# Optimization experiments

Measured on AMD Instinct MI355X. Metric: run time of the kernel, lower is better.

The kernel has to match this reference:

```python
import jax, jax.numpy as jnp
import numpy as np
from jax import lax

S, L = 8192, 16
N_WORD, N_CHAR = 50000, 128
WORD_DIM, CHAR_DIM = 256, 64
WORD_HID, CHAR_HID = 512, 128
N_TAG = 64


def _lstm_gates(x, h, Wih, Whh, bih, bhh):
    # x: [..., D], h: [..., H]; torch gate order: i, f, g, o
    g = x @ Wih.T + h @ Whh.T + bih + bhh
    i, f, gg, o = jnp.split(g, 4, axis=-1)
    return jax.nn.sigmoid(i), jax.nn.sigmoid(f), jnp.tanh(gg), jax.nn.sigmoid(o)


def setup_inputs() -> dict:
    key = jax.random.key(0)
    ks = jax.random.split(key, 16)
    sc = 0.1
    inp = {
        'x': jax.random.randint(ks[0], (S,), 0, N_WORD),
        'chars': jax.random.randint(ks[1], (S, L), 0, N_CHAR),
        'lengths': jax.random.randint(ks[2], (S,), 0, L),
        'word_emb': jax.random.normal(ks[3], (N_WORD, WORD_DIM), jnp.float32) * sc,
        'char_emb': jax.random.normal(ks[4], (N_CHAR, CHAR_DIM), jnp.float32) * sc,
        'c_Wih': jax.random.normal(ks[5], (4 * CHAR_HID, CHAR_DIM), jnp.float32) * sc,
        'c_Whh': jax.random.normal(ks[6], (4 * CHAR_HID, CHAR_HID), jnp.float32) * sc,
        'c_bih': jax.random.normal(ks[7], (4 * CHAR_HID,), jnp.float32) * sc,
        'c_bhh': jax.random.normal(ks[8], (4 * CHAR_HID,), jnp.float32) * sc,
        'w_Wih': jax.random.normal(ks[9], (4 * WORD_HID, WORD_DIM + CHAR_HID), jnp.float32) * sc,
        'w_Whh': jax.random.normal(ks[10], (4 * WORD_HID, WORD_HID), jnp.float32) * sc,
        'w_bih': jax.random.normal(ks[11], (4 * WORD_HID,), jnp.float32) * sc,
        'w_bhh': jax.random.normal(ks[12], (4 * WORD_HID,), jnp.float32) * sc,
        'lin_W': jax.random.normal(ks[13], (N_TAG, WORD_HID), jnp.float32) * sc,
        'lin_b': jax.random.normal(ks[14], (N_TAG,), jnp.float32) * sc,
    }
    return inp


def _char_features(chars, lengths, char_emb, Wih, Whh, bih, bhh):
    # batched char LSTM over all S words at once; returns final CELL state (h[1] in torch)
    emb = char_emb[chars]              # [S, L, char_dim]
    xs = jnp.swapaxes(emb, 0, 1)       # [L, S, char_dim]
    h0 = jnp.zeros((chars.shape[0], CHAR_HID), emb.dtype)
    c0 = jnp.zeros_like(h0)

    def step(carry, inp):
        h, c = carry
        x_t, t = inp
        i, f, g, o = _lstm_gates(x_t, h, Wih, Whh, bih, bhh)
        c_new = f * c + i * g
        h_new = o * jnp.tanh(c_new)
        m = (t < lengths)[:, None]     # only update within each word's true length
        return (jnp.where(m, h_new, h), jnp.where(m, c_new, c)), None

    (h, c), _ = lax.scan(step, (h0, c0), (xs, jnp.arange(L)))
    return c                            # [S, char_hidden]


def _word_lstm(seq, Wih, Whh, bih, bhh):
    # seq: [S, D] single sequence (batch=1 in original)
    h0 = jnp.zeros((WORD_HID,), seq.dtype)
    c0 = jnp.zeros_like(h0)

    def step(carry, x_t):
        h, c = carry
        i, f, g, o = _lstm_gates(x_t, h, Wih, Whh, bih, bhh)
        c = f * c + i * g
        h = o * jnp.tanh(c)
        return (h, c), h

    _, hs = lax.scan(step, (h0, c0), seq)
    return hs                           # [S, word_hidden]


def reference(x, chars, lengths, word_emb, char_emb,
              c_Wih, c_Whh, c_bih, c_bhh,
              w_Wih, w_Whh, w_bih, w_bhh,
              lin_W, lin_b):
    char_feat = _char_features(chars, lengths, char_emb, c_Wih, c_Whh, c_bih, c_bhh)
    we = word_emb[x]                                    # [S, word_dim]
    seq = jnp.concatenate([we, char_feat], axis=1)      # [S, word_dim+char_hidden]
    hs = _word_lstm(seq, w_Wih, w_Whh, w_bih, w_bhh)    # [S, word_hidden]
    logits = hs @ lin_W.T + lin_b                       # [S, n_tag]
    return jax.nn.log_softmax(logits, axis=1)
```

## Files before the change

kernel.cpp:

```cpp
#include <hip/hip_runtime.h>
#include <hip/hip_bf16.h>

#define S_LEN 8192
#define CLEN 16
#define WDIM 256
#define CDIM 64
#define CHID 128
#define WHID 512
#define GDIM 2048
#define NTAG 64
#define KDIM 384
#define NWG 32

typedef unsigned long long u64;

__device__ __forceinline__ float sigmoidf_(float x) {
  return 1.0f / (1.0f + __expf(-x));
}
__device__ __forceinline__ float tanhf_(float x) {
  return 1.0f - 2.0f / (__expf(2.0f * x) + 1.0f);
}

__global__ __launch_bounds__(256)
void char_lstm_kernel(const int* __restrict__ chars, const int* __restrict__ lengths,
                      const float* __restrict__ emb, const float* __restrict__ Wih,
                      const float* __restrict__ Whh, const float* __restrict__ bih,
                      const float* __restrict__ bhh, float* __restrict__ cf)
{
  __shared__ float xs[16][CDIM];
  __shared__ float hsm[16][CHID];
  __shared__ int cidx[16];
  __shared__ int lens[16];
  const int tid = threadIdx.x;
  const int grp = tid >> 7;
  const int j = tid & 127;
  const int wb = blockIdx.x * 16;

  for (int i = tid; i < 16 * CHID; i += 256) (&hsm[0][0])[i] = 0.f;
  if (tid < 16) lens[tid] = lengths[wb + tid];
  float c[8];
#pragma unroll
  for (int w = 0; w < 8; ++w) c[w] = 0.f;
  const float bi = bih[j] + bhh[j];
  const float bf = bih[CHID + j] + bhh[CHID + j];
  const float bg = bih[2 * CHID + j] + bhh[2 * CHID + j];
  const float bo = bih[3 * CHID + j] + bhh[3 * CHID + j];

  for (int t = 0; t < CLEN; ++t) {
    __syncthreads();
    if (tid < 16) cidx[tid] = chars[(wb + tid) * CLEN + t];
    __syncthreads();
    {
      int e = tid * 4;
      int wi = e >> 6;
      int k = e & 63;
      const float4 v = *(const float4*)(emb + (size_t)cidx[wi] * CDIM + k);
      *(float4*)(&xs[wi][k]) = v;
    }
    __syncthreads();
    float ai[8], af[8], ag[8], ao[8];
#pragma unroll
    for (int w = 0; w < 8; ++w) { ai[w] = bi; af[w] = bf; ag[w] = bg; ao[w] = bo; }
    for (int k = 0; k < CDIM; k += 4) {
      float4 w0 = *(const float4*)(Wih + (size_t)j * CDIM + k);
      float4 w1 = *(const float4*)(Wih + (size_t)(CHID + j) * CDIM + k);
      float4 w2 = *(const float4*)(Wih + (size_t)(2 * CHID + j) * CDIM + k);
      float4 w3 = *(const float4*)(Wih + (size_t)(3 * CHID + j) * CDIM + k);
#pragma unroll
      for (int s = 0; s < 4; ++s) {
        float wiv = (&w0.x)[s], wfv = (&w1.x)[s], wgv = (&w2.x)[s], wov = (&w3.x)[s];
#pragma unroll
        for (int w = 0; w < 8; ++w) {
          float xv = xs[grp * 8 + w][k + s];
          ai[w] = fmaf(wiv, xv, ai[w]);
          af[w] = fmaf(wfv, xv, af[w]);
          ag[w] = fmaf(wgv, xv, ag[w]);
          ao[w] = fmaf(wov, xv, ao[w]);
        }
      }
    }
    for (int k = 0; k < CHID; k += 4) {
      float4 w0 = *(const float4*)(Whh + (size_t)j * CHID + k);
      float4 w1 = *(const float4*)(Whh + (size_t)(CHID + j) * CHID + k);
      float4 w2 = *(const float4*)(Whh + (size_t)(2 * CHID + j) * CHID + k);
      float4 w3 = *(const float4*)(Whh + (size_t)(3 * CHID + j) * CHID + k);
#pragma unroll
      for (int s = 0; s < 4; ++s) {
        float wiv = (&w0.x)[s], wfv = (&w1.x)[s], wgv = (&w2.x)[s], wov = (&w3.x)[s];
#pragma unroll
        for (int w = 0; w < 8; ++w) {
          float hv = hsm[grp * 8 + w][k + s];
          ai[w] = fmaf(wiv, hv, ai[w]);
          af[w] = fmaf(wfv, hv, af[w]);
          ag[w] = fmaf(wgv, hv, ag[w]);
          ao[w] = fmaf(wov, hv, ao[w]);
        }
      }
    }
    __syncthreads();
#pragma unroll
    for (int w = 0; w < 8; ++w) {
      if (t < lens[grp * 8 + w]) {
        float iv = sigmoidf_(ai[w]);
        float fv = sigmoidf_(af[w]);
        float gv = tanhf_(ag[w]);
        float ov = sigmoidf_(ao[w]);
        c[w] = fv * c[w] + iv * gv;
        hsm[grp * 8 + w][j] = ov * tanhf_(c[w]);
      }
    }
  }
#pragma unroll
  for (int w = 0; w < 8; ++w)
    cf[(size_t)(wb + grp * 8 + w) * CHID + j] = c[w];
}

#define BM 64
#define BN 64
#define BK 32
__global__ __launch_bounds__(256)
void gx_gemm_kernel(const int* __restrict__ x, const float* __restrict__ word_emb,
                    const float* __restrict__ char_feat, const float* __restrict__ Wih,
                    const float* __restrict__ bih, const float* __restrict__ bhh,
                    float* __restrict__ Gx)
{
  __shared__ float As[BK][BM + 1];
  __shared__ float Bs[BK][BN + 1];
  __shared__ int xidx[BM];
  const int tid = threadIdx.x;
  const int tx = tid & 15, ty = tid >> 4;
  const int m0 = blockIdx.y * BM;
  const int n0 = blockIdx.x * BN;
  if (tid < BM) xidx[tid] = x[m0 + tid];
  float acc[4][4] = {};
  for (int k0 = 0; k0 < KDIM; k0 += BK) {
    __syncthreads();
    {
      int i = tid >> 5;
      int kk = tid & 31;
#pragma unroll
      for (int l = 0; l < 8; ++l) {
        int row = i + l * 8;
        int k = k0 + kk;
        int tt = m0 + row;
        float v = (k < WDIM) ? word_emb[(size_t)xidx[row] * WDIM + k]
                             : char_feat[(size_t)tt * CHID + (k - WDIM)];
        As[kk][row] = v;
      }
    }
    {
      int jjj = tid >> 5;
      int kk = tid & 31;
#pragma unroll
      for (int l = 0; l < 8; ++l) {
        int col = jjj + l * 8;
        Bs[kk][col] = Wih[(size_t)(n0 + col) * KDIM + k0 + kk];
      }
    }
    __syncthreads();
#pragma unroll
    for (int kk = 0; kk < BK; ++kk) {
      float a[4], b[4];
#pragma unroll
      for (int m = 0; m < 4; ++m) a[m] = As[kk][ty * 4 + m];
#pragma unroll
      for (int n = 0; n < 4; ++n) b[n] = Bs[kk][tx * 4 + n];
#pragma unroll
      for (int m = 0; m < 4; ++m)
#pragma unroll
        for (int n = 0; n < 4; ++n)
          acc[m][n] = fmaf(a[m], b[n], acc[m][n]);
    }
  }
#pragma unroll
  for (int n = 0; n < 4; ++n) {
    int g = n0 + tx * 4 + n;
    float bias = bih[g] + bhh[g];
#pragma unroll
    for (int m = 0; m < 4; ++m) {
      int tt = m0 + ty * 4 + m;
      Gx[(size_t)tt * GDIM + g] = acc[m][n] + bias;
    }
  }
}

__global__ __launch_bounds__(256, 1)
void word_lstm_seq(const float* __restrict__ Whh, const float* __restrict__ Gx,
                   float* __restrict__ hs, u64* hbuf)
{
  extern __shared__ float4 wlds4[];
  __shared__ float h_lds[WHID];
  __shared__ float red[2][256];
  const int tid  = threadIdx.x;
  const int wg   = blockIdx.x;
  const int cc   = tid >> 6;
  const int lane = tid & 63;
  const int kb   = cc * 128;
  const int grow = (lane >> 4) * WHID + wg * 16 + (lane & 15);

  for (int L = tid; L < 8192; L += 256) {
    int c2  = L >> 11;
    int rem = L & 2047;
    int j   = rem >> 6;
    int r   = rem & 63;
    int gr  = (r >> 4) * WHID + wg * 16 + (r & 15);
    wlds4[L] = *(const float4*)(Whh + (size_t)gr * WHID + c2 * 128 + 4 * j);
  }
  __syncthreads();

  float c_state = 0.f;

  for (int t = 0; t < S_LEN; ++t) {
    const int par = t & 1;
    float gxv = 0.f;
    if (tid < 64)
      gxv = Gx[(size_t)t * GDIM + grow];
    float v0 = 0.f, v1 = 0.f;
    if (t > 0) {
      const u64* ps = hbuf + (size_t)par * WHID + kb + 2 * lane;
      const unsigned want = (unsigned)t;
      u64 a, b;
      do {
        a = __hip_atomic_load(ps + 0, __ATOMIC_RELAXED, __HIP_MEMORY_SCOPE_AGENT);
        b = __hip_atomic_load(ps + 1, __ATOMIC_RELAXED, __HIP_MEMORY_SCOPE_AGENT);
      } while (((unsigned)(a >> 32) != want) | ((unsigned)(b >> 32) != want));
      v0 = __uint_as_float((unsigned)a);
      v1 = __uint_as_float((unsigned)b);
    }
    *(float2*)(&h_lds[kb + 2 * lane]) = make_float2(v0, v1);
    __threadfence_block();
    const float4* wp = wlds4 + cc * 2048;
    float acc = 0.f;
#pragma unroll
    for (int j = 0; j < 32; ++j) {
      const float4 wv = wp[j * 64 + lane];
      const float4 hv = *(const float4*)(&h_lds[kb + 4 * j]);
      acc = fmaf(wv.x, hv.x, acc);
      acc = fmaf(wv.y, hv.y, acc);
      acc = fmaf(wv.z, hv.z, acc);
      acc = fmaf(wv.w, hv.w, acc);
    }
    red[par][tid] = acc;
    __syncthreads();
    if (tid < 64) {
      const float* rp = red[par];
      float s = rp[tid] + rp[64 + tid] + rp[128 + tid] + rp[192 + tid] + gxv;
      float act = ((tid >> 4) == 2) ? tanhf_(s) : sigmoidf_(s);
      int jj = tid & 15;
      float iv = __shfl(act, jj);
      float fv = __shfl(act, 16 + jj);
      float gv = __shfl(act, 32 + jj);
      float ov = __shfl(act, 48 + jj);
      if (tid < 16) {
        c_state = fv * c_state + iv * gv;
        float hv = ov * tanhf_(c_state);
        const int hidx = wg * 16 + tid;
        const u64 pkt = ((u64)(unsigned)(t + 1) << 32) | (u64)__float_as_uint(hv);
        (void)__hip_atomic_exchange(&hbuf[(size_t)((t + 1) & 1) * WHID + hidx],
                                    pkt, __ATOMIC_RELAXED,
                                    __HIP_MEMORY_SCOPE_AGENT);
        hs[(size_t)t * WHID + hidx] = hv;
      }
    }
  }
}

__global__ __launch_bounds__(256)
void tag_kernel(const float* __restrict__ hs, const float* __restrict__ W,
                const float* __restrict__ b, float* __restrict__ out)
{
  const int wave = threadIdx.x >> 6;
  const int lane = threadIdx.x & 63;
  const int t = blockIdx.x * 4 + wave;
  const float* hr = hs + (size_t)t * WHID;
  const float* wr = W + (size_t)lane * WHID;
  float acc = b[lane];
  for (int k = 0; k < WHID; k += 4) {
    float4 wv = *(const float4*)(wr + k);
    float4 hv = *(const float4*)(hr + k);
    acc = fmaf(wv.x, hv.x, acc);
    acc = fmaf(wv.y, hv.y, acc);
    acc = fmaf(wv.z, hv.z, acc);
    acc = fmaf(wv.w, hv.w, acc);
  }
  float m = acc;
#pragma unroll
  for (int off = 32; off > 0; off >>= 1) m = fmaxf(m, __shfl_xor(m, off));
  float e = __expf(acc - m);
  float sum = e;
#pragma unroll
  for (int off = 32; off > 0; off >>= 1) sum += __shfl_xor(sum, off);
  out[(size_t)t * NTAG + lane] = (acc - m) - __logf(sum);
}

extern "C" void kernel_launch(void* const* d_in, const int* in_sizes, int n_in,
                              void* d_out, int out_size, void* d_ws, size_t ws_size,
                              hipStream_t stream)
{
  const int* x          = (const int*)d_in[0];
  const int* chars      = (const int*)d_in[1];
  const int* lengths    = (const int*)d_in[2];
  const float* word_emb = (const float*)d_in[3];
  const float* char_emb = (const float*)d_in[4];
  const float* c_Wih    = (const float*)d_in[5];
  const float* c_Whh    = (const float*)d_in[6];
  const float* c_bih    = (const float*)d_in[7];
  const float* c_bhh    = (const float*)d_in[8];
  const float* w_Wih    = (const float*)d_in[9];
  const float* w_Whh    = (const float*)d_in[10];
  const float* w_bih    = (const float*)d_in[11];
  const float* w_bhh    = (const float*)d_in[12];
  const float* lin_W    = (const float*)d_in[13];
  const float* lin_b    = (const float*)d_in[14];
  float* out = (float*)d_out;

  char* ws = (char*)d_ws;
  u64*   hbuf      = (u64*)ws;
  float* char_feat = (float*)(ws + 8192);
  float* Gx        = (float*)(ws + 8192 + (size_t)S_LEN * CHID * 4);
  float* hs        = (float*)(ws + 8192 + (size_t)S_LEN * CHID * 4
                                        + (size_t)S_LEN * GDIM * 4);

  hipMemsetAsync(ws, 0, 8192, stream);

  char_lstm_kernel<<<S_LEN / 16, 256, 0, stream>>>(
      chars, lengths, char_emb, c_Wih, c_Whh, c_bih, c_bhh, char_feat);

  dim3 g2(GDIM / BN, S_LEN / BM);
  gx_gemm_kernel<<<g2, 256, 0, stream>>>(
      x, word_emb, char_feat, w_Wih, w_bih, w_bhh, Gx);

  hipFuncSetAttribute((const void*)word_lstm_seq,
                      hipFuncAttributeMaxDynamicSharedMemorySize, 131072);
  word_lstm_seq<<<NWG, 256, 131072, stream>>>(w_Whh, Gx, hs, hbuf);

  tag_kernel<<<S_LEN / 4, 256, 0, stream>>>(hs, lin_W, lin_b, out);
}
```

Before: 17.10 ms.

## Fuse input projection into word LSTM recurrence with register-resident weights

Removes the separate Gx GEMM kernel and its large intermediate buffer. The sequential word LSTM kernel now computes the input projection per timestep itself, gathering the word embedding and char feature into LDS. Both Whh and Wih slices are held in registers (224 floats per thread) instead of LDS. This avoids a full GEMM plus the Gx write/read, but adds per-step global loads and extra FMAs on the serial critical path, and risks register spills.

```diff
diff --git a/kernel.cpp b/kernel.cpp
--- a/kernel.cpp
+++ b/kernel.cpp
@@ -115,106 +115,52 @@
     cf[(size_t)(wb + grp * 8 + w) * CHID + j] = c[w];
 }
 
-#define BM 64
-#define BN 64
-#define BK 32
-__global__ __launch_bounds__(256)
-void gx_gemm_kernel(const int* __restrict__ x, const float* __restrict__ word_emb,
-                    const float* __restrict__ char_feat, const float* __restrict__ Wih,
-                    const float* __restrict__ bih, const float* __restrict__ bhh,
-                    float* __restrict__ Gx)
-{
-  __shared__ float As[BK][BM + 1];
-  __shared__ float Bs[BK][BN + 1];
-  __shared__ int xidx[BM];
-  const int tid = threadIdx.x;
-  const int tx = tid & 15, ty = tid >> 4;
-  const int m0 = blockIdx.y * BM;
-  const int n0 = blockIdx.x * BN;
-  if (tid < BM) xidx[tid] = x[m0 + tid];
-  float acc[4][4] = {};
-  for (int k0 = 0; k0 < KDIM; k0 += BK) {
-    __syncthreads();
-    {
-      int i = tid >> 5;
-      int kk = tid & 31;
-#pragma unroll
-      for (int l = 0; l < 8; ++l) {
-        int row = i + l * 8;
-        int k = k0 + kk;
-        int tt = m0 + row;
-        float v = (k < WDIM) ? word_emb[(size_t)xidx[row] * WDIM + k]
-                             : char_feat[(size_t)tt * CHID + (k - WDIM)];
-        As[kk][row] = v;
-      }
-    }
-    {
-      int jjj = tid >> 5;
-      int kk = tid & 31;
-#pragma unroll
-      for (int l = 0; l < 8; ++l) {
-        int col = jjj + l * 8;
-        Bs[kk][col] = Wih[(size_t)(n0 + col) * KDIM + k0 + kk];
-      }
-    }
-    __syncthreads();
-#pragma unroll
-    for (int kk = 0; kk < BK; ++kk) {
-      float a[4], b[4];
-#pragma unroll
-      for (int m = 0; m < 4; ++m) a[m] = As[kk][ty * 4 + m];
-#pragma unroll
-      for (int n = 0; n < 4; ++n) b[n] = Bs[kk][tx * 4 + n];
-#pragma unroll
-      for (int m = 0; m < 4; ++m)
-#pragma unroll
-        for (int n = 0; n < 4; ++n)
-          acc[m][n] = fmaf(a[m], b[n], acc[m][n]);
-    }
-  }
-#pragma unroll
-  for (int n = 0; n < 4; ++n) {
-    int g = n0 + tx * 4 + n;
-    float bias = bih[g] + bhh[g];
-#pragma unroll
-    for (int m = 0; m < 4; ++m) {
-      int tt = m0 + ty * 4 + m;
-      Gx[(size_t)tt * GDIM + g] = acc[m][n] + bias;
-    }
-  }
-}
-
 __global__ __launch_bounds__(256, 1)
-void word_lstm_seq(const float* __restrict__ Whh, const float* __restrict__ Gx,
+void word_lstm_seq(const float* __restrict__ Whh, const float* __restrict__ Wih,
+                   const float* __restrict__ bih, const float* __restrict__ bhh,
+                   const int* __restrict__ x, const float* __restrict__ word_emb,
+                   const float* __restrict__ cf,
                    float* __restrict__ hs, u64* hbuf)
 {
-  extern __shared__ float4 wlds4[];
   __shared__ float h_lds[WHID];
+  __shared__ float x_lds[KDIM];
   __shared__ float red[2][256];
   const int tid  = threadIdx.x;
   const int wg   = blockIdx.x;
   const int cc   = tid >> 6;
   const int lane = tid & 63;
   const int kb   = cc * 128;
+  const int xb   = cc * 96;
   const int grow = (lane >> 4) * WHID + wg * 16 + (lane & 15);
 
-  for (int L = tid; L < 8192; L += 256) {
-    int c2  = L >> 11;
-    int rem = L & 2047;
-    int j   = rem >> 6;
-    int r   = rem & 63;
-    int gr  = (r >> 4) * WHID + wg * 16 + (r & 15);
-    wlds4[L] = *(const float4*)(Whh + (size_t)gr * WHID + c2 * 128 + 4 * j);
-  }
-  __syncthreads();
+  float wl[128];
+  {
+    const float* wsrc = Whh + (size_t)grow * WHID + kb;
+#pragma unroll
+    for (int k = 0; k < 128; ++k) wl[k] = wsrc[k];
+  }
+  float wx[96];
+  {
+    const float* wsrc = Wih + (size_t)grow * KDIM + xb;
+#pragma unroll
+    for (int k = 0; k < 96; ++k) wx[k] = wsrc[k];
+  }
+  const float bias = bih[grow] + bhh[grow];
 
   float c_state = 0.f;
 
   for (int t = 0; t < S_LEN; ++t) {
     const int par = t & 1;
-    float gxv = 0.f;
-    if (tid < 64)
-      gxv = Gx[(size_t)t * GDIM + grow];
+    {
+      const int xt = x[t];
+      if (lane < 24) {
+        const int gk = xb + 4 * lane;
+        float4 v = (gk < WDIM)
+            ? *(const float4*)(word_emb + (size_t)xt * WDIM + gk)
+            : *(const float4*)(cf + (size_t)t * CHID + (gk - WDIM));
+        *(float4*)(&x_lds[gk]) = v;
+      }
+    }
     float v0 = 0.f, v1 = 0.f;
     if (t > 0) {
       const u64* ps = hbuf + (size_t)par * WHID + kb + 2 * lane;
@@ -229,22 +175,28 @@
     }
     *(float2*)(&h_lds[kb + 2 * lane]) = make_float2(v0, v1);
     __threadfence_block();
-    const float4* wp = wlds4 + cc * 2048;
     float acc = 0.f;
 #pragma unroll
-    for (int j = 0; j < 32; ++j) {
-      const float4 wv = wp[j * 64 + lane];
-      const float4 hv = *(const float4*)(&h_lds[kb + 4 * j]);
-      acc = fmaf(wv.x, hv.x, acc);
-      acc = fmaf(wv.y, hv.y, acc);
-      acc = fmaf(wv.z, hv.z, acc);
-      acc = fmaf(wv.w, hv.w, acc);
+    for (int g = 0; g < 32; ++g) {
+      float4 hv = *(const float4*)(&h_lds[kb + 4 * g]);
+      acc = fmaf(wl[4 * g + 0], hv.x, acc);
+      acc = fmaf(wl[4 * g + 1], hv.y, acc);
+      acc = fmaf(wl[4 * g + 2], hv.z, acc);
+      acc = fmaf(wl[4 * g + 3], hv.w, acc);
+    }
+#pragma unroll
+    for (int g = 0; g < 24; ++g) {
+      float4 xv = *(const float4*)(&x_lds[xb + 4 * g]);
+      acc = fmaf(wx[4 * g + 0], xv.x, acc);
+      acc = fmaf(wx[4 * g + 1], xv.y, acc);
+      acc = fmaf(wx[4 * g + 2], xv.z, acc);
+      acc = fmaf(wx[4 * g + 3], xv.w, acc);
     }
     red[par][tid] = acc;
     __syncthreads();
     if (tid < 64) {
       const float* rp = red[par];
-      float s = rp[tid] + rp[64 + tid] + rp[128 + tid] + rp[192 + tid] + gxv;
+      float s = rp[tid] + rp[64 + tid] + rp[128 + tid] + rp[192 + tid] + bias;
       float act = ((tid >> 4) == 2) ? tanhf_(s) : sigmoidf_(s);
       int jj = tid & 15;
       float iv = __shfl(act, jj);
@@ -317,22 +269,15 @@
   char* ws = (char*)d_ws;
   u64*   hbuf      = (u64*)ws;
   float* char_feat = (float*)(ws + 8192);
-  float* Gx        = (float*)(ws + 8192 + (size_t)S_LEN * CHID * 4);
-  float* hs        = (float*)(ws + 8192 + (size_t)S_LEN * CHID * 4
-                                        + (size_t)S_LEN * GDIM * 4);
+  float* hs        = (float*)(ws + 8192 + (size_t)S_LEN * CHID * 4);
 
   hipMemsetAsync(ws, 0, 8192, stream);
 
   char_lstm_kernel<<<S_LEN / 16, 256, 0, stream>>>(
       chars, lengths, char_emb, c_Wih, c_Whh, c_bih, c_bhh, char_feat);
 
-  dim3 g2(GDIM / BN, S_LEN / BM);
-  gx_gemm_kernel<<<g2, 256, 0, stream>>>(
-      x, word_emb, char_feat, w_Wih, w_bih, w_bhh, Gx);
-
-  hipFuncSetAttribute((const void*)word_lstm_seq,
-                      hipFuncAttributeMaxDynamicSharedMemorySize, 131072);
-  word_lstm_seq<<<NWG, 256, 131072, stream>>>(w_Whh, Gx, hs, hbuf);
+  word_lstm_seq<<<NWG, 256, 0, stream>>>(w_Whh, w_Wih, w_bih, w_bhh,
+                                         x, word_emb, char_feat, hs, hbuf);
 
   tag_kernel<<<S_LEN / 4, 256, 0, stream>>>(hs, lin_W, lin_b, out);
 }
```

Measured after the change: 19.46 ms. 1.14x slower.

## Keep Whh in registers, fuse tag projection into recurrent kernel, drop memset

Applied to the files above, without the earlier changes.

Moves each thread's 128 recurrent weights from LDS into registers, which removes the per-step LDS weight reads. The h vector is now double-buffered in LDS. The separate tag/log-softmax kernel is folded into the sequential word LSTM: idle waves in a rotating workgroup compute the previous step's logits from the shared h, and the last workgroup handles the final step. The hbuf memset is moved into the char LSTM kernel. The risks are register pressure from the 128-float array and extra global reads of lin_W on the latency-critical loop.

```diff
diff --git a/kernel.cpp b/kernel.cpp
--- a/kernel.cpp
+++ b/kernel.cpp
@@ -25,7 +25,8 @@
 void char_lstm_kernel(const int* __restrict__ chars, const int* __restrict__ lengths,
                       const float* __restrict__ emb, const float* __restrict__ Wih,
                       const float* __restrict__ Whh, const float* __restrict__ bih,
-                      const float* __restrict__ bhh, float* __restrict__ cf)
+                      const float* __restrict__ bhh, float* __restrict__ cf,
+                      u64* hbuf)
 {
   __shared__ float xs[16][CDIM];
   __shared__ float hsm[16][CHID];
@@ -35,6 +36,10 @@
   const int grp = tid >> 7;
   const int j = tid & 127;
   const int wb = blockIdx.x * 16;
+
+  if (blockIdx.x == 0) {
+    for (int i = tid; i < 2 * WHID; i += 256) hbuf[i] = 0ULL;
+  }
 
   for (int i = tid; i < 16 * CHID; i += 256) (&hsm[0][0])[i] = 0.f;
   if (tid < 16) lens[tid] = lengths[wb + tid];
@@ -186,10 +191,10 @@
 
 __global__ __launch_bounds__(256, 1)
 void word_lstm_seq(const float* __restrict__ Whh, const float* __restrict__ Gx,
-                   float* __restrict__ hs, u64* hbuf)
+                   const float* __restrict__ linW, const float* __restrict__ linb,
+                   float* __restrict__ out, u64* hbuf)
 {
-  extern __shared__ float4 wlds4[];
-  __shared__ float h_lds[WHID];
+  __shared__ float h_lds[2][WHID];
   __shared__ float red[2][256];
   const int tid  = threadIdx.x;
   const int wg   = blockIdx.x;
@@ -198,15 +203,12 @@
   const int kb   = cc * 128;
   const int grow = (lane >> 4) * WHID + wg * 16 + (lane & 15);
 
-  for (int L = tid; L < 8192; L += 256) {
-    int c2  = L >> 11;
-    int rem = L & 2047;
-    int j   = rem >> 6;
-    int r   = rem & 63;
-    int gr  = (r >> 4) * WHID + wg * 16 + (r & 15);
-    wlds4[L] = *(const float4*)(Whh + (size_t)gr * WHID + c2 * 128 + 4 * j);
-  }
-  __syncthreads();
+  float wl[128];
+  {
+    const float* wsrc = Whh + (size_t)grow * WHID + kb;
+#pragma unroll
+    for (int k = 0; k < 128; ++k) wl[k] = wsrc[k];
+  }
 
   float c_state = 0.f;
 
@@ -227,18 +229,16 @@
       v0 = __uint_as_float((unsigned)a);
       v1 = __uint_as_float((unsigned)b);
     }
-    *(float2*)(&h_lds[kb + 2 * lane]) = make_float2(v0, v1);
+    *(float2*)(&h_lds[par][kb + 2 * lane]) = make_float2(v0, v1);
     __threadfence_block();
-    const float4* wp = wlds4 + cc * 2048;
     float acc = 0.f;
 #pragma unroll
-    for (int j = 0; j < 32; ++j) {
-      const float4 wv = wp[j * 64 + lane];
-      const float4 hv = *(const float4*)(&h_lds[kb + 4 * j]);
-      acc = fmaf(wv.x, hv.x, acc);
-      acc = fmaf(wv.y, hv.y, acc);
-      acc = fmaf(wv.z, hv.z, acc);
-      acc = fmaf(wv.w, hv.w, acc);
+    for (int g = 0; g < 32; ++g) {
+      float4 hv = *(const float4*)(&h_lds[par][kb + 4 * g]);
+      acc = fmaf(wl[4 * g + 0], hv.x, acc);
+      acc = fmaf(wl[4 * g + 1], hv.y, acc);
+      acc = fmaf(wl[4 * g + 2], hv.z, acc);
+      acc = fmaf(wl[4 * g + 3], hv.w, acc);
     }
     red[par][tid] = acc;
     __syncthreads();
@@ -259,38 +259,62 @@
         (void)__hip_atomic_exchange(&hbuf[(size_t)((t + 1) & 1) * WHID + hidx],
                                     pkt, __ATOMIC_RELAXED,
                                     __HIP_MEMORY_SCOPE_AGENT);
-        hs[(size_t)t * WHID + hidx] = hv;
-      }
-    }
-  }
-}
-
-__global__ __launch_bounds__(256)
-void tag_kernel(const float* __restrict__ hs, const float* __restrict__ W,
-                const float* __restrict__ b, float* __restrict__ out)
-{
-  const int wave = threadIdx.x >> 6;
-  const int lane = threadIdx.x & 63;
-  const int t = blockIdx.x * 4 + wave;
-  const float* hr = hs + (size_t)t * WHID;
-  const float* wr = W + (size_t)lane * WHID;
-  float acc = b[lane];
-  for (int k = 0; k < WHID; k += 4) {
-    float4 wv = *(const float4*)(wr + k);
-    float4 hv = *(const float4*)(hr + k);
-    acc = fmaf(wv.x, hv.x, acc);
-    acc = fmaf(wv.y, hv.y, acc);
-    acc = fmaf(wv.z, hv.z, acc);
-    acc = fmaf(wv.w, hv.w, acc);
-  }
-  float m = acc;
-#pragma unroll
-  for (int off = 32; off > 0; off >>= 1) m = fmaxf(m, __shfl_xor(m, off));
-  float e = __expf(acc - m);
-  float sum = e;
-#pragma unroll
-  for (int off = 32; off > 0; off >>= 1) sum += __shfl_xor(sum, off);
-  out[(size_t)t * NTAG + lane] = (acc - m) - __logf(sum);
+      }
+    } else if (t > 0 && ((t - 1) & 31) == wg &&
+               cc == 1 + (((t - 1) >> 5) % 3)) {
+      const float* hrow = h_lds[par];
+      const float* wrow = linW + (size_t)lane * WHID;
+      float a2 = linb[lane];
+      for (int k = 0; k < WHID; k += 4) {
+        float4 wv = *(const float4*)(wrow + k);
+        a2 = fmaf(wv.x, hrow[k + 0], a2);
+        a2 = fmaf(wv.y, hrow[k + 1], a2);
+        a2 = fmaf(wv.z, hrow[k + 2], a2);
+        a2 = fmaf(wv.w, hrow[k + 3], a2);
+      }
+      float m = a2;
+#pragma unroll
+      for (int off = 32; off > 0; off >>= 1) m = fmaxf(m, __shfl_xor(m, off));
+      float e = __expf(a2 - m);
+      float sum = e;
+#pragma unroll
+      for (int off = 32; off > 0; off >>= 1) sum += __shfl_xor(sum, off);
+      out[(size_t)(t - 1) * NTAG + lane] = (a2 - m) - __logf(sum);
+    }
+  }
+
+  if (wg == 31) {
+    const u64* ps = hbuf + kb + 2 * lane;
+    const unsigned want = (unsigned)S_LEN;
+    u64 a, b;
+    do {
+      a = __hip_atomic_load(ps + 0, __ATOMIC_RELAXED, __HIP_MEMORY_SCOPE_AGENT);
+      b = __hip_atomic_load(ps + 1, __ATOMIC_RELAXED, __HIP_MEMORY_SCOPE_AGENT);
+    } while (((unsigned)(a >> 32) != want) | ((unsigned)(b >> 32) != want));
+    *(float2*)(&h_lds[0][kb + 2 * lane]) =
+        make_float2(__uint_as_float((unsigned)a), __uint_as_float((unsigned)b));
+    __syncthreads();
+    if (tid < 64) {
+      const float* hrow = h_lds[0];
+      const float* wrow = linW + (size_t)tid * WHID;
+      float a2 = linb[tid];
+      for (int k = 0; k < WHID; k += 4) {
+        float4 wv = *(const float4*)(wrow + k);
+        a2 = fmaf(wv.x, hrow[k + 0], a2);
+        a2 = fmaf(wv.y, hrow[k + 1], a2);
+        a2 = fmaf(wv.z, hrow[k + 2], a2);
+        a2 = fmaf(wv.w, hrow[k + 3], a2);
+      }
+      float m = a2;
+#pragma unroll
+      for (int off = 32; off > 0; off >>= 1) m = fmaxf(m, __shfl_xor(m, off));
+      float e = __expf(a2 - m);
+      float sum = e;
+#pragma unroll
+      for (int off = 32; off > 0; off >>= 1) sum += __shfl_xor(sum, off);
+      out[(size_t)(S_LEN - 1) * NTAG + tid] = (a2 - m) - __logf(sum);
+    }
+  }
 }
 
 extern "C" void kernel_launch(void* const* d_in, const int* in_sizes, int n_in,
@@ -318,21 +342,13 @@
   u64*   hbuf      = (u64*)ws;
   float* char_feat = (float*)(ws + 8192);
   float* Gx        = (float*)(ws + 8192 + (size_t)S_LEN * CHID * 4);
-  float* hs        = (float*)(ws + 8192 + (size_t)S_LEN * CHID * 4
-                                        + (size_t)S_LEN * GDIM * 4);
-
-  hipMemsetAsync(ws, 0, 8192, stream);
 
   char_lstm_kernel<<<S_LEN / 16, 256, 0, stream>>>(
-      chars, lengths, char_emb, c_Wih, c_Whh, c_bih, c_bhh, char_feat);
+      chars, lengths, char_emb, c_Wih, c_Whh, c_bih, c_bhh, char_feat, hbuf);
 
   dim3 g2(GDIM / BN, S_LEN / BM);
   gx_gemm_kernel<<<g2, 256, 0, stream>>>(
       x, word_emb, char_feat, w_Wih, w_bih, w_bhh, Gx);
 
-  hipFuncSetAttribute((const void*)word_lstm_seq,
-                      hipFuncAttributeMaxDynamicSharedMemorySize, 131072);
-  word_lstm_seq<<<NWG, 256, 131072, stream>>>(w_Whh, Gx, hs, hbuf);
-
-  tag_kernel<<<S_LEN / 4, 256, 0, stream>>>(hs, lin_W, lin_b, out);
-}
+  word_lstm_seq<<<NWG, 256, 0, stream>>>(w_Whh, Gx, lin_W, lin_b, out, hbuf);
+}
```

Measured after the change: 35.97 ms. 110% more time.
